# Kernel optimization log

Measured on AMD Instinct MI355X. Metric: run time of the kernel, lower is better.

The kernel has to match this reference:

```python
import jax, jax.numpy as jnp
import numpy as np
import math

N_HEAD = 16
N_CTX = 1024


def setup_inputs() -> dict:
    key = jax.random.key(0)
    ks = jax.random.split(key, 3)
    B, S, NX = 4, 1024, 1024
    x = jax.random.normal(ks[0], (B, S, NX), dtype=jnp.float32)
    # Conv1D weights stored as [nx, nf], init std=0.02, bias zeros
    c_attn_w = jax.random.normal(ks[1], (NX, 3 * NX), dtype=jnp.float32) * 0.02
    c_attn_b = jnp.zeros((3 * NX,), dtype=jnp.float32)
    c_proj_w = jax.random.normal(ks[2], (NX, NX), dtype=jnp.float32) * 0.02
    c_proj_b = jnp.zeros((NX,), dtype=jnp.float32)
    return {"x": x, "c_attn_w": c_attn_w, "c_attn_b": c_attn_b,
            "c_proj_w": c_proj_w, "c_proj_b": c_proj_b}


def reference(x, c_attn_w, c_attn_b, c_proj_w, c_proj_b):
    B, S, NX = x.shape
    H = N_HEAD
    D = NX // H
    # c_attn: Conv1D -> x @ W + b, then split into q, k, v
    qkv = x @ c_attn_w + c_attn_b                      # [B,S,3*NX]
    q, k, v = jnp.split(qkv, 3, axis=-1)               # each [B,S,NX]
    # split heads: q,v -> [B,H,S,D]; k -> [B,H,D,S]
    q = q.reshape(B, S, H, D).transpose(0, 2, 1, 3)
    k = k.reshape(B, S, H, D).transpose(0, 2, 3, 1)
    v = v.reshape(B, S, H, D).transpose(0, 2, 1, 3)
    # _attn: scores, scale, combined multiplicative+additive causal mask, softmax
    w = jnp.matmul(q, k)                               # [B,H,S,S]
    w = w / math.sqrt(D)                               # scale=True
    bias = jnp.tril(jnp.ones((S, S), dtype=w.dtype))[None, None]  # causal tril slice
    w = w * bias - 1e10 * (1.0 - bias)
    w = jax.nn.softmax(w, axis=-1)
    a = jnp.matmul(w, v)                               # [B,H,S,D]
    # merge heads
    a = a.transpose(0, 2, 1, 3).reshape(B, S, NX)
    # c_proj
    return a @ c_proj_w + c_proj_b
```

## Files before the change

kernel.cpp:

```cpp
#include <hip/hip_runtime.h>
#include <cstdint>

typedef __attribute__((ext_vector_type(8))) short short8;
typedef __attribute__((ext_vector_type(4))) short short4x;
typedef __attribute__((ext_vector_type(4))) float floatx4;

__device__ __forceinline__ unsigned short f2b(float f) {
    unsigned int u = __builtin_bit_cast(unsigned int, f);
    u += 0x7fffu + ((u >> 16) & 1u);
    return (unsigned short)(u >> 16);
}
__device__ __forceinline__ float b2f(unsigned short s) {
    unsigned int u = ((unsigned int)s) << 16;
    return __builtin_bit_cast(float, u);
}
__device__ __forceinline__ float fast_exp2(float x) {
    float r;
    asm("v_exp_f32 %0, %1" : "=v"(r) : "v"(x));
    return r;
}
__device__ __forceinline__ unsigned int pack_bf16_trunc(float lo, float hi) {
    return __builtin_amdgcn_perm(__builtin_bit_cast(unsigned int, hi),
                                 __builtin_bit_cast(unsigned int, lo), 0x07060302u);
}

#define GLDS(g, l) __builtin_amdgcn_global_load_lds(                                   \
    (const __attribute__((address_space(1))) unsigned int*)(g),                        \
    (__attribute__((address_space(3))) unsigned int*)(l), 16, 0, 0)

__global__ __launch_bounds__(256) void prep_kernel(const float* __restrict__ x,
                                                   unsigned short* __restrict__ xb,
                                                   const float* __restrict__ w1,
                                                   unsigned short* __restrict__ w1t,
                                                   const float* __restrict__ w2,
                                                   unsigned short* __restrict__ w2t) {
    __shared__ unsigned short tile[64][65];
    const int b = blockIdx.x, t = threadIdx.x;
    if (b < 1024) {
        for (int i = b * 256 + t; i < 1048576; i += 262144) {
            float4 v = ((const float4*)x)[i];
            ushort4 o;
            o.x = f2b(v.x); o.y = f2b(v.y); o.z = f2b(v.z); o.w = f2b(v.w);
            ((ushort4*)xb)[i] = o;
        }
        return;
    }
    const float* W; unsigned short* Wt; int K, N, kb, nb;
    if (b < 1792) { W = w1; Wt = w1t; K = 1024; N = 3072; kb = (b - 1024) & 15; nb = (b - 1024) >> 4; }
    else          { W = w2; Wt = w2t; K = 1024; N = 1024; kb = (b - 1792) & 15; nb = (b - 1792) >> 4; }
    const int k0 = kb * 64, n0 = nb * 64;
    for (int idx = t; idx < 64 * 64; idx += 256) {
        int i = idx >> 6, j = idx & 63;
        tile[j][i] = f2b(W[(size_t)(k0 + i) * N + n0 + j]);
    }
    __syncthreads();
    for (int idx = t; idx < 64 * 64; idx += 256) {
        int r = idx >> 6, c = idx & 63;
        Wt[(size_t)(n0 + r) * K + k0 + c] = tile[r][c];
    }
}

#define MFMA16(a_, b_, c_) __builtin_amdgcn_mfma_f32_16x16x32_bf16((a_), (b_), (c_), 0, 0, 0)

#define GBSTAGE(kt_, bf_) {                                             \
    const unsigned short* sa_ = aSrc + (kt_) * 32;                      \
    const unsigned short* sb_ = bSrc + (kt_) * 32;                      \
    GLDS(sa_,             &As[bf_][ldsOff]);                            \
    GLDS(sa_ + 64 * 1024, &As[bf_][2048 + ldsOff]);                     \
    GLDS(sb_,             &Bs[bf_][ldsOff]);                            \
    GLDS(sb_ + 64 * 1024, &Bs[bf_][2048 + ldsOff]); }

__global__ __launch_bounds__(256) void gemm_bt_kernel(const unsigned short* __restrict__ A,
                                                      const unsigned short* __restrict__ Bt,
                                                      const float* __restrict__ bias,
                                                      unsigned short* __restrict__ C,
                                                      unsigned short* __restrict__ vTout,
                                                      int vSplit) {
    __shared__ unsigned short As[3][128 * 32];
    __shared__ unsigned short Bs[3][128 * 32];

    const int t = threadIdx.x;
    const int wave = t >> 6, lane = t & 63;
    const int quad = lane >> 4, l16 = lane & 15;
    const int rowBase = blockIdx.x << 7;
    const int colBase = blockIdx.y << 7;
    const int waveM = (wave >> 1) * 64;
    const int waveN = (wave & 1) * 64;

    floatx4 acc[4][4];
#pragma unroll
    for (int i = 0; i < 4; ++i)
#pragma unroll
        for (int j = 0; j < 4; ++j) acc[i][j] = (floatx4){0.f, 0.f, 0.f, 0.f};

    const int rr = t >> 2;
    const int gsrc = ((t & 3) ^ (rr & 3)) * 8;
    const unsigned short* aSrc = A + (size_t)(rowBase + rr) * 1024 + gsrc;
    const unsigned short* bSrc = Bt + (size_t)(colBase + rr) * 1024 + gsrc;
    const int ldsOff = t * 8;

    const int g0 = (quad ^ (l16 & 3)) * 8;
    const int aOff = (waveM + l16) * 32 + g0;
    const int bOff = (waveN + l16) * 32 + g0;

    GBSTAGE(0, 0);
    GBSTAGE(1, 1);

    int bufR = 0, bufS = 2;
    for (int kt = 0; kt < 32; ++kt) {
        if (kt < 31) asm volatile("s_waitcnt vmcnt(4)" ::: "memory");
        else         asm volatile("s_waitcnt vmcnt(0)" ::: "memory");
        __builtin_amdgcn_s_barrier();
        if (kt + 2 < 32) GBSTAGE(kt + 2, bufS);

        const unsigned short* Ab = &As[bufR][0];
        const unsigned short* Bb = &Bs[bufR][0];
        short8 af[4], bf[4];
#pragma unroll
        for (int mi = 0; mi < 4; ++mi) af[mi] = *(const short8*)&Ab[aOff + mi * 512];
#pragma unroll
        for (int ni = 0; ni < 4; ++ni) bf[ni] = *(const short8*)&Bb[bOff + ni * 512];
        asm volatile("s_waitcnt lgkmcnt(0)" ::: "memory");
        __builtin_amdgcn_sched_barrier(0);
        __builtin_amdgcn_s_setprio(1);
#pragma unroll
        for (int mi = 0; mi < 4; ++mi)
#pragma unroll
            for (int ni = 0; ni < 4; ++ni)
                acc[mi][ni] = MFMA16(af[mi], bf[ni], acc[mi][ni]);
        __builtin_amdgcn_s_setprio(0);

        bufR = (bufR == 2) ? 0 : bufR + 1;
        bufS = (bufS == 2) ? 0 : bufS + 1;
    }

    if (colBase >= vSplit) {
#pragma unroll
        for (int mi = 0; mi < 4; ++mi)
#pragma unroll
            for (int ni = 0; ni < 4; ++ni) {
                int col = colBase + waveN + ni * 16 + l16 - vSplit;
                float bv = bias[colBase + waveN + ni * 16 + l16];
#pragma unroll
                for (int r = 0; r < 4; ++r) {
                    int row = rowBase + waveM + mi * 16 + quad * 4 + r;
                    vTout[((size_t)((row >> 10) * 16 + (col >> 6)) * 64 + (col & 63)) * 1024
                          + (row & 1023)] = f2b(acc[mi][ni][r] + bv);
                }
            }
    } else {
#pragma unroll
        for (int mi = 0; mi < 4; ++mi)
#pragma unroll
            for (int ni = 0; ni < 4; ++ni) {
                int col = colBase + waveN + ni * 16 + l16;
                float bv = bias[col];
#pragma unroll
                for (int r = 0; r < 4; ++r) {
                    int row = rowBase + waveM + mi * 16 + quad * 4 + r;
                    C[(size_t)row * 3072 + col] = f2b(acc[mi][ni][r] + bv);
                }
            }
    }
}

#define G2LDA(mi, kc) (*(const short8*)&As2[buf][aRow + (mi) * 1024 + ((kc) ? g1 : g0)])
#define G2LDB(ni, kc) (*(const short8*)&Bs2[buf][bRow + (ni) * 1024 + ((kc) ? g1 : g0)])
#define G2STAGE(kt_) { const unsigned short* sa_ = aSrc + (kt_) * 64;   \
    const unsigned short* sb_ = bSrc + (kt_) * 64;                      \
    GLDS(sa_,              &As2[(kt_) & 1][ldsOff]);                    \
    GLDS(sa_ + 64 * 1024,  &As2[(kt_) & 1][4096 + ldsOff]);             \
    GLDS(sb_,              &Bs2[(kt_) & 1][ldsOff]);                    \
    GLDS(sb_ + 64 * 1024,  &Bs2[(kt_) & 1][4096 + ldsOff]); }

__global__ __launch_bounds__(512, 2) void gemm2_kernel(const unsigned short* __restrict__ A,
                                                       const unsigned short* __restrict__ Bt,
                                                       const float* __restrict__ bias,
                                                       float* __restrict__ C) {
    __shared__ unsigned short As2[2][128 * 64];
    __shared__ unsigned short Bs2[2][128 * 64];

    const int t = threadIdx.x;
    const int wave = t >> 6, lane = t & 63;
    const int quad = lane >> 4, l16 = lane & 15;
    const int wm = wave >> 2, wn = wave & 3;
    const int rowBase = blockIdx.x << 7;
    const int colBase = blockIdx.y << 7;

    floatx4 acc[4][2];
#pragma unroll
    for (int i = 0; i < 4; ++i)
#pragma unroll
        for (int j = 0; j < 2; ++j) acc[i][j] = (floatx4){0.f, 0.f, 0.f, 0.f};

    const int rr = t >> 3;
    const int gsrc = ((t & 7) ^ (rr & 7)) * 8;
    const unsigned short* aSrc = A + (size_t)(rowBase + rr) * 1024 + gsrc;
    const unsigned short* bSrc = Bt + (size_t)(colBase + rr) * 1024 + gsrc;
    const int ldsOff = t * 8;

    const int rg = l16 & 7;
    const int g0 = (quad ^ rg) * 8;
    const int g1 = g0 ^ 32;
    const int aRow = (wm * 64 + l16) * 64;
    const int bRow = (wn * 32 + l16) * 64;

    G2STAGE(0);

    for (int kt = 0; kt < 16; ++kt) {
        const int buf = kt & 1;
        asm volatile("s_waitcnt vmcnt(0)" ::: "memory");
        __builtin_amdgcn_s_barrier();
        if (kt + 1 < 16) G2STAGE(kt + 1);

        short8 a0k0 = G2LDA(0, 0), a0k1 = G2LDA(0, 1);
        short8 a1k0 = G2LDA(1, 0), a1k1 = G2LDA(1, 1);
        short8 a2k0 = G2LDA(2, 0), a2k1 = G2LDA(2, 1);
        short8 a3k0 = G2LDA(3, 0), a3k1 = G2LDA(3, 1);
        short8 b0k0 = G2LDB(0, 0), b0k1 = G2LDB(0, 1);
        short8 b1k0 = G2LDB(1, 0), b1k1 = G2LDB(1, 1);
        asm volatile("s_waitcnt lgkmcnt(0)" ::: "memory");
        __builtin_amdgcn_sched_barrier(0);
        __builtin_amdgcn_s_setprio(1);
        acc[0][0] = MFMA16(a0k0, b0k0, acc[0][0]);
        acc[1][0] = MFMA16(a1k0, b0k0, acc[1][0]);
        acc[2][0] = MFMA16(a2k0, b0k0, acc[2][0]);
        acc[3][0] = MFMA16(a3k0, b0k0, acc[3][0]);
        acc[0][1] = MFMA16(a0k0, b1k0, acc[0][1]);
        acc[1][1] = MFMA16(a1k0, b1k0, acc[1][1]);
        acc[2][1] = MFMA16(a2k0, b1k0, acc[2][1]);
        acc[3][1] = MFMA16(a3k0, b1k0, acc[3][1]);
        acc[0][0] = MFMA16(a0k1, b0k1, acc[0][0]);
        acc[1][0] = MFMA16(a1k1, b0k1, acc[1][0]);
        acc[2][0] = MFMA16(a2k1, b0k1, acc[2][0]);
        acc[3][0] = MFMA16(a3k1, b0k1, acc[3][0]);
        acc[0][1] = MFMA16(a0k1, b1k1, acc[0][1]);
        acc[1][1] = MFMA16(a1k1, b1k1, acc[1][1]);
        acc[2][1] = MFMA16(a2k1, b1k1, acc[2][1]);
        acc[3][1] = MFMA16(a3k1, b1k1, acc[3][1]);
        __builtin_amdgcn_s_setprio(0);
    }

#pragma unroll
    for (int mi = 0; mi < 4; ++mi)
#pragma unroll
        for (int ni = 0; ni < 2; ++ni) {
            int col = colBase + wn * 32 + ni * 16 + l16;
            float bv = bias[col];
#pragma unroll
            for (int r = 0; r < 4; ++r) {
                int row = rowBase + wm * 64 + mi * 16 + quad * 4 + r;
                C[(size_t)row * 1024 + col] = acc[mi][ni][r] + bv;
            }
        }
}

__global__ __launch_bounds__(256) void attn_kernel(const unsigned short* __restrict__ qkv,
                                                   const unsigned short* __restrict__ vT,
                                                   unsigned short* __restrict__ aout) {
    __shared__ unsigned short Ks[2][2][4096];
    __shared__ unsigned short Vs[2][2][4096];
    __shared__ unsigned short Tb[4][16 * 72];

    const int p  = blockIdx.x;
    const int bh = blockIdx.y;
    const int b = bh >> 4, h = bh & 15;
    const int qb1 = p, qb2 = 15 - p;
    const int t = threadIdx.x;
    const int wave = t >> 6, lane = t & 63;
    const int quad = lane >> 4, l16 = lane & 15;
    const int h7 = l16 & 7;

    const size_t rowB = (size_t)b * 1024;
    const size_t hoff = (size_t)h * 64;
    const int qA0 = qb1 * 64 + wave * 16;
    const int qB0 = qb2 * 64 + wave * 16;

    const float qscale = 0.125f * 1.44269504f;
    short8 qfA[2], qfB[2];
#pragma unroll
    for (int kc = 0; kc < 2; ++kc) {
        short8 qa = *(const short8*)(qkv + (rowB + qA0 + l16) * 3072 + hoff + kc * 32 + quad * 8);
        short8 qb = *(const short8*)(qkv + (rowB + qB0 + l16) * 3072 + hoff + kc * 32 + quad * 8);
#pragma unroll
        for (int e = 0; e < 8; ++e) {
            qa[e] = (short)f2b(b2f((unsigned short)qa[e]) * qscale);
            qb[e] = (short)f2b(b2f((unsigned short)qb[e]) * qscale);
        }
        qfA[kc] = qa; qfB[kc] = qb;
    }

    const int lr = lane >> 3;
    const int sc8 = (lane & 7) * 8;
    const int gc8 = ((lane & 7) ^ lr) * 8;
    const unsigned short* kSrc = qkv + rowB * 3072 + hoff + 1024;
    const unsigned short* vSrc = vT + (size_t)bh * 65536;

    auto stageT = [&](int kt, int bf, int sl) {
        const unsigned short* kp = kSrc + (size_t)kt * 64 * 3072;
        const unsigned short* vp = vSrc + kt * 64;
        int r0 = wave * 16 + lr, r1 = r0 + 8;
        GLDS(kp + (size_t)r0 * 3072 + gc8, &Ks[bf][sl][r0 * 64 + sc8]);
        GLDS(kp + (size_t)r1 * 3072 + gc8, &Ks[bf][sl][r1 * 64 + sc8]);
        GLDS(vp + (size_t)r0 * 1024 + gc8, &Vs[bf][sl][r0 * 64 + sc8]);
        GLDS(vp + (size_t)r1 * 1024 + gc8, &Vs[bf][sl][r1 * 64 + sc8]);
    };

    float lpA = 0.f, lpB = 0.f;
    floatx4 oA[4], oB[4];
#pragma unroll
    for (int ni = 0; ni < 4; ++ni) {
        oA[ni] = (floatx4){0.f, 0.f, 0.f, 0.f};
        oB[ni] = (floatx4){0.f, 0.f, 0.f, 0.f};
    }

    const int nT = qb2 + 1;
    const int nP = (nT + 1) >> 1;

    auto doTile = [&](int kt, const unsigned short* Kb, const unsigned short* Vb) {
        short8 kf[4][2];
#pragma unroll
        for (int jn = 0; jn < 4; ++jn)
#pragma unroll
            for (int kc = 0; kc < 2; ++kc)
                kf[jn][kc] = *(const short8*)&Kb[(jn * 16 + l16) * 64 + (((kc * 4 + quad) ^ h7) * 8)];
        short4x vf[4][4];
#pragma unroll
        for (int ni = 0; ni < 4; ++ni)
#pragma unroll
            for (int jb = 0; jb < 4; ++jb)
                vf[ni][jb] = *(const short4x*)&Vb[(ni * 16 + l16) * 64 +
                                                 (((jb * 2 + (quad >> 1)) ^ h7) * 8) + (quad & 1) * 4];

        auto qtile = [&](short8 (&qf)[2], floatx4 (&o)[4], float& lp, bool diag) {
            floatx4 s[4];
#pragma unroll
            for (int jn = 0; jn < 4; ++jn) s[jn] = (floatx4){0.f, 0.f, 0.f, 0.f};
#pragma unroll
            for (int jn = 0; jn < 4; ++jn)
#pragma unroll
                for (int kc = 0; kc < 2; ++kc)
                    s[jn] = __builtin_amdgcn_mfma_f32_16x16x32_bf16(kf[jn][kc], qf[kc], s[jn], 0, 0, 0);
            if (diag) {
                int ql = wave * 16 + l16;
#pragma unroll
                for (int jn = 0; jn < 4; ++jn)
#pragma unroll
                    for (int r = 0; r < 4; ++r)
                        if (jn * 16 + quad * 4 + r > ql) s[jn][r] = -1e30f;
            }
            short4x pb[4];
#pragma unroll
            for (int jb = 0; jb < 4; ++jb) {
                float pe0 = fast_exp2(s[jb][0]);
                float pe1 = fast_exp2(s[jb][1]);
                float pe2 = fast_exp2(s[jb][2]);
                float pe3 = fast_exp2(s[jb][3]);
                lp += (pe0 + pe1) + (pe2 + pe3);
                uint2 u;
                u.x = pack_bf16_trunc(pe0, pe1);
                u.y = pack_bf16_trunc(pe2, pe3);
                pb[jb] = __builtin_bit_cast(short4x, u);
            }
#pragma unroll
            for (int jb = 0; jb < 4; ++jb)
#pragma unroll
                for (int ni = 0; ni < 4; ++ni)
                    o[ni] = __builtin_amdgcn_mfma_f32_16x16x16bf16_1k(vf[ni][jb], pb[jb], o[ni], 0, 0, 0);
        };

        qtile(qfB, oB, lpB, kt == qb2);
        if (kt <= qb1) qtile(qfA, oA, lpA, kt == qb1);
    };

    stageT(0, 0, 0);
    stageT(1, 0, 1);

    for (int pi = 0; pi < nP; ++pi) {
        __syncthreads();
        if (pi + 1 < nP) {
            stageT(2 * pi + 2, (pi + 1) & 1, 0);
            if (2 * pi + 3 < nT) stageT(2 * pi + 3, (pi + 1) & 1, 1);
        }
        const int bfI = pi & 1;
        doTile(2 * pi, &Ks[bfI][0][0], &Vs[bfI][0][0]);
        if (2 * pi + 1 < nT) doTile(2 * pi + 1, &Ks[bfI][1][0], &Vs[bfI][1][0]);
    }

    lpA += __shfl_xor(lpA, 16); lpA += __shfl_xor(lpA, 32);
    lpB += __shfl_xor(lpB, 16); lpB += __shfl_xor(lpB, 32);
    const float liA = 1.f / lpA, liB = 1.f / lpB;

    auto writeOut = [&](floatx4 (&o)[4], float li, int q0) {
#pragma unroll
        for (int ni = 0; ni < 4; ++ni)
#pragma unroll
            for (int r = 0; r < 4; ++r)
                Tb[wave][l16 * 72 + ni * 16 + quad * 4 + r] = f2b(o[ni][r] * li);
#pragma unroll
        for (int i = 0; i < 2; ++i) {
            int q = lane >> 2, c = (lane & 3) + 4 * i;
            short8 v = *(const short8*)&Tb[wave][q * 72 + c * 8];
            *(short8*)(aout + (rowB + q0 + q) * 1024 + hoff + c * 8) = v;
        }
    };
    writeOut(oA, liA, qA0);
    writeOut(oB, liB, qB0);
}

extern "C" void kernel_launch(void* const* d_in, const int* in_sizes, int n_in,
                              void* d_out, int out_size, void* d_ws, size_t ws_size,
                              hipStream_t stream) {
    const float* x  = (const float*)d_in[0];
    const float* w1 = (const float*)d_in[1];
    const float* b1 = (const float*)d_in[2];
    const float* w2 = (const float*)d_in[3];
    const float* b2 = (const float*)d_in[4];
    float* out = (float*)d_out;

    unsigned short* xb   = (unsigned short*)d_ws;
    unsigned short* w1t  = xb  + (size_t)4096 * 1024;
    unsigned short* w2t  = w1t + (size_t)3072 * 1024;
    unsigned short* qkv  = w2t + (size_t)1024 * 1024;
    unsigned short* attn = qkv + (size_t)4096 * 3072;
    unsigned short* vTb  = attn + (size_t)4096 * 1024;

    prep_kernel<<<2048, 256, 0, stream>>>(x, xb, w1, w1t, w2, w2t);
    gemm_bt_kernel<<<dim3(32, 24), 256, 0, stream>>>(xb, w1t, b1, qkv, vTb, 2048);
    attn_kernel<<<dim3(8, 64), 256, 0, stream>>>(qkv, vTb, attn);
    gemm2_kernel<<<dim3(32, 8), 512, 0, stream>>>(attn, w2t, b2, out);
}
```

Measured before the change: 175.8 us.

## Simplify QKV GEMM to double-buffered unswizzled staging and vectorize vT stores

The QKV GEMM main loop drops the triple-buffered pipeline, which used explicit vmcnt waits, an XOR-swizzled LDS layout, s_setprio and sched_barrier. In its place is a plain double-buffered loop with __syncthreads and row-major [128][32] LDS tiles, with M/N/K passed as parameters. Separately, the transposed-V epilogue now packs four bf16 values into one 8-byte store instead of four scalar stores. The packed store should cut write instructions. The unswizzled LDS reads will likely hit bank conflicts, and the shallower prefetch exposes more global latency. Correctness also depends on __syncthreads waiting for the async LDS loads to finish.

```diff
diff --git a/kernel.cpp b/kernel.cpp
--- a/kernel.cpp
+++ b/kernel.cpp
@@ -62,28 +62,21 @@
 
 #define MFMA16(a_, b_, c_) __builtin_amdgcn_mfma_f32_16x16x32_bf16((a_), (b_), (c_), 0, 0, 0)
 
-#define GBSTAGE(kt_, bf_) {                                             \
-    const unsigned short* sa_ = aSrc + (kt_) * 32;                      \
-    const unsigned short* sb_ = bSrc + (kt_) * 32;                      \
-    GLDS(sa_,             &As[bf_][ldsOff]);                            \
-    GLDS(sa_ + 64 * 1024, &As[bf_][2048 + ldsOff]);                     \
-    GLDS(sb_,             &Bs[bf_][ldsOff]);                            \
-    GLDS(sb_ + 64 * 1024, &Bs[bf_][2048 + ldsOff]); }
-
 __global__ __launch_bounds__(256) void gemm_bt_kernel(const unsigned short* __restrict__ A,
                                                       const unsigned short* __restrict__ Bt,
                                                       const float* __restrict__ bias,
                                                       unsigned short* __restrict__ C,
                                                       unsigned short* __restrict__ vTout,
-                                                      int vSplit) {
-    __shared__ unsigned short As[3][128 * 32];
-    __shared__ unsigned short Bs[3][128 * 32];
+                                                      int vSplit,
+                                                      int M, int N, int K) {
+    __shared__ unsigned short As[2][128][32];
+    __shared__ unsigned short Bs[2][128][32];
 
     const int t = threadIdx.x;
     const int wave = t >> 6, lane = t & 63;
     const int quad = lane >> 4, l16 = lane & 15;
-    const int rowBase = blockIdx.x << 7;
-    const int colBase = blockIdx.y << 7;
+    const int rowBase = blockIdx.x * 128;
+    const int colBase = blockIdx.y * 128;
     const int waveM = (wave >> 1) * 64;
     const int waveN = (wave & 1) * 64;
 
@@ -93,45 +86,39 @@
 #pragma unroll
         for (int j = 0; j < 4; ++j) acc[i][j] = (floatx4){0.f, 0.f, 0.f, 0.f};
 
-    const int rr = t >> 2;
-    const int gsrc = ((t & 3) ^ (rr & 3)) * 8;
-    const unsigned short* aSrc = A + (size_t)(rowBase + rr) * 1024 + gsrc;
-    const unsigned short* bSrc = Bt + (size_t)(colBase + rr) * 1024 + gsrc;
-    const int ldsOff = t * 8;
-
-    const int g0 = (quad ^ (l16 & 3)) * 8;
-    const int aOff = (waveM + l16) * 32 + g0;
-    const int bOff = (waveN + l16) * 32 + g0;
-
-    GBSTAGE(0, 0);
-    GBSTAGE(1, 1);
-
-    int bufR = 0, bufS = 2;
-    for (int kt = 0; kt < 32; ++kt) {
-        if (kt < 31) asm volatile("s_waitcnt vmcnt(4)" ::: "memory");
-        else         asm volatile("s_waitcnt vmcnt(0)" ::: "memory");
-        __builtin_amdgcn_s_barrier();
-        if (kt + 2 < 32) GBSTAGE(kt + 2, bufS);
-
-        const unsigned short* Ab = &As[bufR][0];
-        const unsigned short* Bb = &Bs[bufR][0];
+    const int r0 = t >> 2, cc0 = (t & 3) * 8;
+    const int r1 = 64 + (t >> 2);
+    const unsigned short* aBase = A + (size_t)rowBase * K;
+    const unsigned short* bBase = Bt + (size_t)colBase * K;
+
+    auto stage = [&](int kk, int bf) {
+        const int k0 = kk * 32;
+        GLDS(aBase + (size_t)r0 * K + k0 + cc0, &As[bf][r0][cc0]);
+        GLDS(aBase + (size_t)r1 * K + k0 + cc0, &As[bf][r1][cc0]);
+        GLDS(bBase + (size_t)r0 * K + k0 + cc0, &Bs[bf][r0][cc0]);
+        GLDS(bBase + (size_t)r1 * K + k0 + cc0, &Bs[bf][r1][cc0]);
+    };
+
+    const int nIter = K >> 5;
+    stage(0, 0);
+
+    for (int kk = 0; kk < nIter; ++kk) {
+        __syncthreads();
+        if (kk + 1 < nIter) stage(kk + 1, (kk + 1) & 1);
+        const int buf = kk & 1;
+
         short8 af[4], bf[4];
 #pragma unroll
-        for (int mi = 0; mi < 4; ++mi) af[mi] = *(const short8*)&Ab[aOff + mi * 512];
-#pragma unroll
-        for (int ni = 0; ni < 4; ++ni) bf[ni] = *(const short8*)&Bb[bOff + ni * 512];
-        asm volatile("s_waitcnt lgkmcnt(0)" ::: "memory");
-        __builtin_amdgcn_sched_barrier(0);
-        __builtin_amdgcn_s_setprio(1);
+        for (int mi = 0; mi < 4; ++mi)
+            af[mi] = *(const short8*)&As[buf][waveM + mi * 16 + l16][quad * 8];
+#pragma unroll
+        for (int ni = 0; ni < 4; ++ni)
+            bf[ni] = *(const short8*)&Bs[buf][waveN + ni * 16 + l16][quad * 8];
 #pragma unroll
         for (int mi = 0; mi < 4; ++mi)
 #pragma unroll
             for (int ni = 0; ni < 4; ++ni)
                 acc[mi][ni] = MFMA16(af[mi], bf[ni], acc[mi][ni]);
-        __builtin_amdgcn_s_setprio(0);
-
-        bufR = (bufR == 2) ? 0 : bufR + 1;
-        bufS = (bufS == 2) ? 0 : bufS + 1;
     }
 
     if (colBase >= vSplit) {
@@ -139,14 +126,20 @@
         for (int mi = 0; mi < 4; ++mi)
 #pragma unroll
             for (int ni = 0; ni < 4; ++ni) {
-                int col = colBase + waveN + ni * 16 + l16 - vSplit;
-                float bv = bias[colBase + waveN + ni * 16 + l16];
-#pragma unroll
-                for (int r = 0; r < 4; ++r) {
-                    int row = rowBase + waveM + mi * 16 + quad * 4 + r;
-                    vTout[((size_t)((row >> 10) * 16 + (col >> 6)) * 64 + (col & 63)) * 1024
-                          + (row & 1023)] = f2b(acc[mi][ni][r] + bv);
-                }
+                int colq = colBase + waveN + ni * 16 + l16;
+                int col = colq - vSplit;
+                float bv = bias[colq];
+                int row0 = rowBase + waveM + mi * 16 + quad * 4;
+                unsigned short e0 = f2b(acc[mi][ni][0] + bv);
+                unsigned short e1 = f2b(acc[mi][ni][1] + bv);
+                unsigned short e2 = f2b(acc[mi][ni][2] + bv);
+                unsigned short e3 = f2b(acc[mi][ni][3] + bv);
+                uint2 uu;
+                uu.x = (unsigned int)e0 | ((unsigned int)e1 << 16);
+                uu.y = (unsigned int)e2 | ((unsigned int)e3 << 16);
+                size_t idx = ((size_t)((row0 >> 10) * 16 + (col >> 6)) * 64 + (col & 63)) * 1024
+                             + (row0 & 1023);
+                *(uint2*)&vTout[idx] = uu;
             }
     } else {
 #pragma unroll
@@ -158,7 +151,7 @@
 #pragma unroll
                 for (int r = 0; r < 4; ++r) {
                     int row = rowBase + waveM + mi * 16 + quad * 4 + r;
-                    C[(size_t)row * 3072 + col] = f2b(acc[mi][ni][r] + bv);
+                    C[(size_t)row * N + col] = f2b(acc[mi][ni][r] + bv);
                 }
             }
     }
@@ -426,7 +419,8 @@
     unsigned short* vTb  = attn + (size_t)4096 * 1024;
 
     prep_kernel<<<2048, 256, 0, stream>>>(x, xb, w1, w1t, w2, w2t);
-    gemm_bt_kernel<<<dim3(32, 24), 256, 0, stream>>>(xb, w1t, b1, qkv, vTb, 2048);
+    gemm_bt_kernel<<<dim3(32, 24), 256, 0, stream>>>(xb, w1t, b1, qkv, vTb, 2048,
+                                                     4096, 3072, 1024);
     attn_kernel<<<dim3(8, 64), 256, 0, stream>>>(qkv, vTb, attn);
     gemm2_kernel<<<dim3(32, 8), 512, 0, stream>>>(attn, w2t, b2, out);
 }
```

Result: no change. 177.1 us (+0.7%).
